# Kernel optimization log

Hardware: AMD Instinct MI355X
Metric: run time of the kernel (lower is better)

The kernel has to match this reference:

```python
import jax, jax.numpy as jnp
import numpy as np

EMB_DIM = 512
NUM_HEADS = 8
HEAD_DIM = EMB_DIM // NUM_HEADS


def setup_inputs() -> dict:
    key = jax.random.key(0)
    ks = jax.random.split(key, 8)
    B, S, D = 2, 192, EMB_DIM
    return {
        "q": jax.random.normal(ks[0], (B, S, D), dtype=jnp.float32),
        "k": jax.random.normal(ks[1], (B, S, D), dtype=jnp.float32),
        "l": jax.random.normal(ks[2], (B, S, D), dtype=jnp.float32),
        "v": jax.random.normal(ks[3], (B, S, D), dtype=jnp.float32),
        "Wq": jax.random.normal(ks[4], (D, D), dtype=jnp.float32) * (1.0 / np.sqrt(D)),
        "Wk": jax.random.normal(ks[5], (D, D), dtype=jnp.float32) * (1.0 / np.sqrt(D)),
        "Wv": jax.random.normal(ks[6], (D, D), dtype=jnp.float32) * (1.0 / np.sqrt(D)),
        "Wout": jax.random.normal(ks[7], (D, D), dtype=jnp.float32) * (1.0 / np.sqrt(D)),
    }


def _heads(x, W):
    # torch nn.Linear: x @ W.T ; then split heads -> (B, H, S, hd)
    B, S, D = x.shape
    y = x @ W.T
    return y.reshape(B, S, NUM_HEADS, HEAD_DIM).transpose(0, 2, 1, 3)


def reference(q, k, l, v, Wq, Wk, Wv, Wout):
    B, QS, D = q.shape
    KS, LS = k.shape[1], l.shape[1]
    qh = _heads(q, Wq)
    kh = _heads(k, Wk)
    lh = _heads(l, Wk)  # NOTE: original module projects l with self.key (faithful)
    vh = _heads(v, Wv)
    # rank-3 attention scores: (B, H, QS, KS, LS)
    scores = jnp.einsum('bhqe,bhke,bhle->bhqkl', qh, kh, lh) / jnp.sqrt(
        jnp.asarray(HEAD_DIM, dtype=q.dtype))
    # softmax jointly over (KS, LS)
    attn = jax.nn.softmax(scores.reshape(B, NUM_HEADS, QS, KS * LS), axis=-1)
    attn = attn.reshape(B, NUM_HEADS, QS, KS, LS)
    # vv[b,h,l,k,d] = v[b,h,k,d]; contract over k and l -> (B, QS, H, hd)
    attended = jnp.einsum('bhqkl,bhkd->bqhd', attn, vh)
    concatenated = attended.reshape(B, QS, EMB_DIM)
    return concatenated @ Wout.T
```

## Files before the change

kernel.cpp:

```cpp
#include <hip/hip_runtime.h>
#include <math.h>

#define BB 2
#define SS 192
#define DD 512
#define HH 8
#define HD 64
#define QCB 6
#define NQC (SS / QCB)
#define PROJ_N (BB*HH*SS*HD)
#define KLPAD (8 * 193 * 8)
#define SCL (0.125f * 1.44269504088896f)

typedef __attribute__((ext_vector_type(4))) float f32x4;
typedef _Float16 f16x8 __attribute__((ext_vector_type(8)));

__device__ __forceinline__ f16x8 cvt8_f16_rne(const float* g) {
    f16x8 r;
#pragma unroll
    for (int i = 0; i < 8; ++i) r[i] = (_Float16)g[i];
    return r;
}
__device__ __forceinline__ short f16s(float v) {
    return __builtin_bit_cast(short, (_Float16)v);
}

__global__ __launch_bounds__(256) void proj4_kernel(
    const float* __restrict__ xq, const float* __restrict__ xk,
    const float* __restrict__ xl, const float* __restrict__ xv,
    const float* __restrict__ Wq, const float* __restrict__ Wk,
    const float* __restrict__ Wv, float* __restrict__ vhp,
    short* __restrict__ qf16, short* __restrict__ khf16,
    short* __restrict__ lhf16, float* __restrict__ out) {
    const int p = blockIdx.z;
    const float* x = (p == 0) ? xq : (p == 1) ? xk : (p == 2) ? xl : xv;
    const float* W = (p == 0) ? Wq : (p == 3) ? Wv : Wk;

    __shared__ short Ahs[2][8 * 64 * 8];
    __shared__ short Bhs[2][8 * 64 * 8];

    const int t = threadIdx.x;

    {
        const int bid = (blockIdx.z * gridDim.y + blockIdx.y) * gridDim.x + blockIdx.x;
        for (int i = bid * 256 + t; i < BB * SS * DD; i += 192 * 256) out[i] = 0.f;
    }

    const int lane = t & 63, w = t >> 6;
    const int wr = w >> 1, wc = w & 1;
    const int c16 = lane & 15, q4 = lane >> 4;
    const int m0 = blockIdx.x * 64, n0 = blockIdx.y * 64;
    const int r = t >> 2, cc = t & 3;

    f32x4 acc[2][2];
#pragma unroll
    for (int a = 0; a < 2; ++a)
#pragma unroll
        for (int b = 0; b < 2; ++b) acc[a][b] = (f32x4){0.f, 0.f, 0.f, 0.f};

#define STAGE(kk, bf)                                                               \
    {                                                                               \
        _Pragma("unroll") for (int h2 = 0; h2 < 2; ++h2) {                          \
            const int ec = cc * 2 + h2;                                             \
            float a8[8], w8[8];                                                     \
            *(f32x4*)&a8[0] = *(const f32x4*)&x[(m0 + r) * 512 + (kk) + ec * 8];    \
            *(f32x4*)&a8[4] = *(const f32x4*)&x[(m0 + r) * 512 + (kk) + ec * 8 + 4];\
            *(f32x4*)&w8[0] = *(const f32x4*)&W[(n0 + r) * 512 + (kk) + ec * 8];    \
            *(f32x4*)&w8[4] = *(const f32x4*)&W[(n0 + r) * 512 + (kk) + ec * 8 + 4];\
            *(f16x8*)&Ahs[bf][(ec * 64 + r) * 8] = cvt8_f16_rne(a8);                \
            *(f16x8*)&Bhs[bf][(ec * 64 + r) * 8] = cvt8_f16_rne(w8);                \
        }                                                                           \
    }

    STAGE(0, 0)
    for (int s = 0; s < 8; ++s) {
        __syncthreads();
        if (s + 1 < 8) STAGE((s + 1) * 64, (s + 1) & 1)
        const int b = s & 1;
        f16x8 aH[2][2], bH[2][2];
#pragma unroll
        for (int mt = 0; mt < 2; ++mt) {
            const int row = wr * 32 + mt * 16 + c16;
            aH[mt][0] = *(const f16x8*)&Ahs[b][(q4 * 64 + row) * 8];
            aH[mt][1] = *(const f16x8*)&Ahs[b][((q4 + 4) * 64 + row) * 8];
        }
#pragma unroll
        for (int nt = 0; nt < 2; ++nt) {
            const int col = wc * 32 + nt * 16 + c16;
            bH[nt][0] = *(const f16x8*)&Bhs[b][(q4 * 64 + col) * 8];
            bH[nt][1] = *(const f16x8*)&Bhs[b][((q4 + 4) * 64 + col) * 8];
        }
#pragma unroll
        for (int mt = 0; mt < 2; ++mt)
#pragma unroll
            for (int nt = 0; nt < 2; ++nt) {
                acc[mt][nt] = __builtin_amdgcn_mfma_f32_16x16x32_f16(aH[mt][0], bH[nt][0], acc[mt][nt], 0, 0, 0);
                acc[mt][nt] = __builtin_amdgcn_mfma_f32_16x16x32_f16(aH[mt][1], bH[nt][1], acc[mt][nt], 0, 0, 0);
            }
    }
#undef STAGE

#pragma unroll
    for (int mt = 0; mt < 2; ++mt)
#pragma unroll
        for (int nt = 0; nt < 2; ++nt)
#pragma unroll
            for (int j = 0; j < 4; ++j) {
                const int n_row = m0 + wr * 32 + mt * 16 + q4 * 4 + j;
                const int col = n0 + wc * 32 + nt * 16 + c16;
                const int b = n_row / SS, s2 = n_row % SS;
                const int h = col >> 6, e = col & 63;
                const int bh = b * HH + h;
                const float v = acc[mt][nt][j];
                if (p == 3) {
                    vhp[(bh * SS + s2) * HD + e] = v;
                } else if (p == 0) {
                    qf16[(bh * SS + s2) * HD + e] = f16s(v * SCL);
                } else {
                    short* dst = (p == 1) ? khf16 : lhf16;
                    dst[bh * KLPAD + (e >> 3) * (193 * 8) + s2 * 8 + (e & 7)] = f16s(v);
                }
            }
}

__global__ __launch_bounds__(512, 4) void attn3d_mfma_kernel(
    const short* __restrict__ qf16, const short* __restrict__ khf16,
    const short* __restrict__ lhf16, const float* __restrict__ vh,
    const float* __restrict__ Wout, float* __restrict__ out) {
    __shared__ short Kf16[8][193][8];
    __shared__ short Lf16[8][193][8];
    __shared__ short qpk[QCB][8][8];
    __shared__ float partial[2][QCB][196];
    __shared__ float Wt[QCB][192];
    __shared__ float attd[16][72];
    __shared__ float zinv[QCB];

    const int blk = blockIdx.x;
    const int bh = blk >> 5, qc = blk & 31;
    const int t = threadIdx.x;
    const int lane = t & 63, w = t >> 6;
    const int lg = w >> 2, kg = w & 3;
    const int c = lane & 15, eh = lane >> 4;

    if (t < QCB * 8) {
        const int q = t >> 3, ecj = t & 7;
        *(f16x8*)&qpk[q][ecj][0] =
            *(const f16x8*)&qf16[(bh * SS + qc * QCB + q) * HD + ecj * 8];
    }
#pragma unroll
    for (int j = 0; j < 3; ++j) {
        const int cid = t + 512 * j;
        const int ec = cid / 192, k2 = cid - ec * 192;
        const int off = ec * (193 * 8) + k2 * 8;
        *(f16x8*)&(((short*)Kf16)[off]) = *(const f16x8*)&khf16[bh * KLPAD + off];
        *(f16x8*)&(((short*)Lf16)[off]) = *(const f16x8*)&lhf16[bh * KLPAD + off];
    }
    __syncthreads();

    for (int qpi = 0; qpi < 3; ++qpi) {
        const int qa = (qpi + w) % 3;
        const int qb = qa + 3;
        const f16x8 qaf0 = *(const f16x8*)&qpk[qa][eh][0];
        const f16x8 qaf1 = *(const f16x8*)&qpk[qa][4 + eh][0];
        const f16x8 qbf0 = *(const f16x8*)&qpk[qb][eh][0];
        const f16x8 qbf1 = *(const f16x8*)&qpk[qb][4 + eh][0];
        f16x8 Ba[3][2], Bb[3][2];
#pragma unroll
        for (int kt = 0; kt < 3; ++kt) {
            const int col = kg * 48 + kt * 16 + c;
            const f16x8 Kf0 = *(const f16x8*)&Kf16[eh][col][0];
            const f16x8 Kf1 = *(const f16x8*)&Kf16[4 + eh][col][0];
            Ba[kt][0] = Kf0 * qaf0;
            Ba[kt][1] = Kf1 * qaf1;
            Bb[kt][0] = Kf0 * qbf0;
            Bb[kt][1] = Kf1 * qbf1;
        }
        float ra0 = 0.f, ra1 = 0.f, ra2 = 0.f;
        float rb0 = 0.f, rb1 = 0.f, rb2 = 0.f;
#pragma unroll
        for (int lt = 0; lt < 6; ++lt) {
            const int row = lg * 96 + lt * 16 + c;
            const f16x8 A0 = *(const f16x8*)&Lf16[eh][row][0];
            const f16x8 A1 = *(const f16x8*)&Lf16[4 + eh][row][0];
            f32x4 a0 = (f32x4){0.f, 0.f, 0.f, 0.f};
            f32x4 a1 = (f32x4){0.f, 0.f, 0.f, 0.f};
            f32x4 a2 = (f32x4){0.f, 0.f, 0.f, 0.f};
            f32x4 b0 = (f32x4){0.f, 0.f, 0.f, 0.f};
            f32x4 b1 = (f32x4){0.f, 0.f, 0.f, 0.f};
            f32x4 b2 = (f32x4){0.f, 0.f, 0.f, 0.f};
            a0 = __builtin_amdgcn_mfma_f32_16x16x32_f16(A0, Ba[0][0], a0, 0, 0, 0);
            a1 = __builtin_amdgcn_mfma_f32_16x16x32_f16(A0, Ba[1][0], a1, 0, 0, 0);
            a2 = __builtin_amdgcn_mfma_f32_16x16x32_f16(A0, Ba[2][0], a2, 0, 0, 0);
            b0 = __builtin_amdgcn_mfma_f32_16x16x32_f16(A0, Bb[0][0], b0, 0, 0, 0);
            b1 = __builtin_amdgcn_mfma_f32_16x16x32_f16(A0, Bb[1][0], b1, 0, 0, 0);
            b2 = __builtin_amdgcn_mfma_f32_16x16x32_f16(A0, Bb[2][0], b2, 0, 0, 0);
            a0 = __builtin_amdgcn_mfma_f32_16x16x32_f16(A1, Ba[0][1], a0, 0, 0, 0);
            a1 = __builtin_amdgcn_mfma_f32_16x16x32_f16(A1, Ba[1][1], a1, 0, 0, 0);
            a2 = __builtin_amdgcn_mfma_f32_16x16x32_f16(A1, Ba[2][1], a2, 0, 0, 0);
            b0 = __builtin_amdgcn_mfma_f32_16x16x32_f16(A1, Bb[0][1], b0, 0, 0, 0);
            b1 = __builtin_amdgcn_mfma_f32_16x16x32_f16(A1, Bb[1][1], b1, 0, 0, 0);
            b2 = __builtin_amdgcn_mfma_f32_16x16x32_f16(A1, Bb[2][1], b2, 0, 0, 0);
            ra0 += (__builtin_amdgcn_exp2f(a0[0]) + __builtin_amdgcn_exp2f(a0[1])) +
                   (__builtin_amdgcn_exp2f(a0[2]) + __builtin_amdgcn_exp2f(a0[3]));
            ra1 += (__builtin_amdgcn_exp2f(a1[0]) + __builtin_amdgcn_exp2f(a1[1])) +
                   (__builtin_amdgcn_exp2f(a1[2]) + __builtin_amdgcn_exp2f(a1[3]));
            ra2 += (__builtin_amdgcn_exp2f(a2[0]) + __builtin_amdgcn_exp2f(a2[1])) +
                   (__builtin_amdgcn_exp2f(a2[2]) + __builtin_amdgcn_exp2f(a2[3]));
            rb0 += (__builtin_amdgcn_exp2f(b0[0]) + __builtin_amdgcn_exp2f(b0[1])) +
                   (__builtin_amdgcn_exp2f(b0[2]) + __builtin_amdgcn_exp2f(b0[3]));
            rb1 += (__builtin_amdgcn_exp2f(b1[0]) + __builtin_amdgcn_exp2f(b1[1])) +
                   (__builtin_amdgcn_exp2f(b1[2]) + __builtin_amdgcn_exp2f(b1[3]));
            rb2 += (__builtin_amdgcn_exp2f(b2[0]) + __builtin_amdgcn_exp2f(b2[1])) +
                   (__builtin_amdgcn_exp2f(b2[2]) + __builtin_amdgcn_exp2f(b2[3]));
        }
        ra0 += __shfl_xor(ra0, 16, 64);
        ra1 += __shfl_xor(ra1, 16, 64);
        ra2 += __shfl_xor(ra2, 16, 64);
        rb0 += __shfl_xor(rb0, 16, 64);
        rb1 += __shfl_xor(rb1, 16, 64);
        rb2 += __shfl_xor(rb2, 16, 64);
        ra0 += __shfl_xor(ra0, 32, 64);
        ra1 += __shfl_xor(ra1, 32, 64);
        ra2 += __shfl_xor(ra2, 32, 64);
        rb0 += __shfl_xor(rb0, 32, 64);
        rb1 += __shfl_xor(rb1, 32, 64);
        rb2 += __shfl_xor(rb2, 32, 64);
        if (eh == 0) {
            partial[lg][qa][kg * 48 + 0 * 16 + c] = ra0;
            partial[lg][qa][kg * 48 + 1 * 16 + c] = ra1;
            partial[lg][qa][kg * 48 + 2 * 16 + c] = ra2;
            partial[lg][qb][kg * 48 + 0 * 16 + c] = rb0;
            partial[lg][qb][kg * 48 + 1 * 16 + c] = rb1;
            partial[lg][qb][kg * 48 + 2 * 16 + c] = rb2;
        }
    }
    __syncthreads();

    for (int id = t; id < QCB * 192; id += 512) {
        const int q = id / 192, k = id - q * 192;
        Wt[q][k] = partial[0][q][k] + partial[1][q][k];
    }
    for (int id = t; id < 16 * 72; id += 512) ((float*)attd)[id] = 0.f;
    __syncthreads();

    if (w < QCB) {
        const int q = w;
        float z = Wt[q][lane] + Wt[q][lane + 64] + Wt[q][lane + 128];
#pragma unroll
        for (int off = 32; off >= 1; off >>= 1) z += __shfl_xor(z, off, 64);
        if (lane == 0) zinv[q] = 1.f / z;
    }
    __syncthreads();

    if (t < QCB * 64) {
        const int q = t >> 6, d = t & 63;
        const float* vp = vh + bh * SS * HD + d;
        float sum = 0.f;
        for (int k0 = 0; k0 < SS; k0 += 8) {
            float v8[8];
#pragma unroll
            for (int j = 0; j < 8; ++j) v8[j] = vp[(k0 + j) * HD];
#pragma unroll
            for (int j = 0; j < 8; ++j) sum = fmaf(Wt[q][k0 + j], v8[j], sum);
        }
        attd[q][d] = sum * zinv[q];
    }
    __syncthreads();

    const int b = bh >> 3, h = bh & 7;
    f16x8 Ae0, Ae1;
    {
        float a8[8];
        *(f32x4*)&a8[0] = *(const f32x4*)&attd[c][eh * 8];
        *(f32x4*)&a8[4] = *(const f32x4*)&attd[c][eh * 8 + 4];
        Ae0 = cvt8_f16_rne(a8);
        *(f32x4*)&a8[0] = *(const f32x4*)&attd[c][32 + eh * 8];
        *(f32x4*)&a8[4] = *(const f32x4*)&attd[c][32 + eh * 8 + 4];
        Ae1 = cvt8_f16_rne(a8);
    }
#pragma unroll
    for (int jt = 0; jt < 4; ++jt) {
        const int j = (w * 4 + jt) * 16 + c;
        const float* wp = &Wout[j * DD + h * HD];
        float b8[8];
        *(f32x4*)&b8[0] = *(const f32x4*)&wp[eh * 8];
        *(f32x4*)&b8[4] = *(const f32x4*)&wp[eh * 8 + 4];
        const f16x8 B0 = cvt8_f16_rne(b8);
        *(f32x4*)&b8[0] = *(const f32x4*)&wp[32 + eh * 8];
        *(f32x4*)&b8[4] = *(const f32x4*)&wp[32 + eh * 8 + 4];
        const f16x8 B1 = cvt8_f16_rne(b8);
        f32x4 oc = (f32x4){0.f, 0.f, 0.f, 0.f};
        oc = __builtin_amdgcn_mfma_f32_16x16x32_f16(Ae0, B0, oc, 0, 0, 0);
        oc = __builtin_amdgcn_mfma_f32_16x16x32_f16(Ae1, B1, oc, 0, 0, 0);
#pragma unroll
        for (int jj = 0; jj < 4; ++jj) {
            const int q = eh * 4 + jj;
            if (q < QCB)
                atomicAdd(&out[(b * SS + qc * QCB + q) * DD + (w * 4 + jt) * 16 + c], oc[jj]);
        }
    }
}

extern "C" void kernel_launch(void* const* d_in, const int* in_sizes, int n_in,
                              void* d_out, int out_size, void* d_ws, size_t ws_size,
                              hipStream_t stream) {
    (void)in_sizes; (void)n_in; (void)out_size; (void)ws_size;
    const float* q    = (const float*)d_in[0];
    const float* k    = (const float*)d_in[1];
    const float* l    = (const float*)d_in[2];
    const float* v    = (const float*)d_in[3];
    const float* Wq   = (const float*)d_in[4];
    const float* Wk   = (const float*)d_in[5];
    const float* Wv   = (const float*)d_in[6];
    const float* Wout = (const float*)d_in[7];
    float* out = (float*)d_out;

    float* ws    = (float*)d_ws;
    float* vhp   = ws;
    short* qf16  = (short*)(ws + PROJ_N);
    short* khf16 = qf16 + PROJ_N;
    short* lhf16 = khf16 + 16 * KLPAD;

    proj4_kernel<<<dim3(384 / 64, 512 / 64, 4), 256, 0, stream>>>(
        q, k, l, v, Wq, Wk, Wv, vhp, qf16, khf16, lhf16, out);
    attn3d_mfma_kernel<<<dim3(16 * NQC), 512, 0, stream>>>(
        qf16, khf16, lhf16, vhp, Wout, out);
}
```

Measured before the change: 42.38 us.

## Split projection K-reduction across two thread teams per block

The projection kernel now runs 512 threads per block, split into two 256-thread teams that each reduce half of the K=512 dimension with their own double-buffered shared tiles. Team 1 writes its partial accumulators to shared memory and team 0 adds them before the usual scatter to the head layouts. The aim is more parallelism and a shorter serial K loop for a grid of only 192 blocks, at the cost of extra shared memory, one additional barrier and the reduction step.

Result: no change. 41.91 us, median of 2 (-1.1%).

```diff
diff --git a/kernel.cpp b/kernel.cpp
--- a/kernel.cpp
+++ b/kernel.cpp
@@ -25,7 +25,7 @@
     return __builtin_bit_cast(short, (_Float16)v);
 }
 
-__global__ __launch_bounds__(256) void proj4_kernel(
+__global__ __launch_bounds__(512) void proj4_kernel(
     const float* __restrict__ xq, const float* __restrict__ xk,
     const float* __restrict__ xl, const float* __restrict__ xv,
     const float* __restrict__ Wq, const float* __restrict__ Wk,
@@ -36,21 +36,24 @@
     const float* x = (p == 0) ? xq : (p == 1) ? xk : (p == 2) ? xl : xv;
     const float* W = (p == 0) ? Wq : (p == 3) ? Wv : Wk;
 
-    __shared__ short Ahs[2][8 * 64 * 8];
-    __shared__ short Bhs[2][8 * 64 * 8];
+    __shared__ short Ahs[2][2][8 * 64 * 8];
+    __shared__ short Bhs[2][2][8 * 64 * 8];
+    __shared__ float accs[64][65];
 
     const int t = threadIdx.x;
 
     {
         const int bid = (blockIdx.z * gridDim.y + blockIdx.y) * gridDim.x + blockIdx.x;
-        for (int i = bid * 256 + t; i < BB * SS * DD; i += 192 * 256) out[i] = 0.f;
-    }
-
-    const int lane = t & 63, w = t >> 6;
-    const int wr = w >> 1, wc = w & 1;
+        for (int i = bid * 512 + t; i < BB * SS * DD; i += 192 * 512) out[i] = 0.f;
+    }
+
+    const int team = t >> 8, tt = t & 255;
+    const int lane = tt & 63, w4 = tt >> 6;
+    const int wr = w4 >> 1, wc = w4 & 1;
     const int c16 = lane & 15, q4 = lane >> 4;
     const int m0 = blockIdx.x * 64, n0 = blockIdx.y * 64;
-    const int r = t >> 2, cc = t & 3;
+    const int r = tt >> 2, cc = tt & 3;
+    const int kbase = team * 256;
 
     f32x4 acc[2][2];
 #pragma unroll
@@ -67,28 +70,28 @@
             *(f32x4*)&a8[4] = *(const f32x4*)&x[(m0 + r) * 512 + (kk) + ec * 8 + 4];\
             *(f32x4*)&w8[0] = *(const f32x4*)&W[(n0 + r) * 512 + (kk) + ec * 8];    \
             *(f32x4*)&w8[4] = *(const f32x4*)&W[(n0 + r) * 512 + (kk) + ec * 8 + 4];\
-            *(f16x8*)&Ahs[bf][(ec * 64 + r) * 8] = cvt8_f16_rne(a8);                \
-            *(f16x8*)&Bhs[bf][(ec * 64 + r) * 8] = cvt8_f16_rne(w8);                \
+            *(f16x8*)&Ahs[team][bf][(ec * 64 + r) * 8] = cvt8_f16_rne(a8);          \
+            *(f16x8*)&Bhs[team][bf][(ec * 64 + r) * 8] = cvt8_f16_rne(w8);          \
         }                                                                           \
     }
 
-    STAGE(0, 0)
-    for (int s = 0; s < 8; ++s) {
+    STAGE(kbase, 0)
+    for (int s = 0; s < 4; ++s) {
         __syncthreads();
-        if (s + 1 < 8) STAGE((s + 1) * 64, (s + 1) & 1)
+        if (s + 1 < 4) STAGE(kbase + (s + 1) * 64, (s + 1) & 1)
         const int b = s & 1;
         f16x8 aH[2][2], bH[2][2];
 #pragma unroll
         for (int mt = 0; mt < 2; ++mt) {
             const int row = wr * 32 + mt * 16 + c16;
-            aH[mt][0] = *(const f16x8*)&Ahs[b][(q4 * 64 + row) * 8];
-            aH[mt][1] = *(const f16x8*)&Ahs[b][((q4 + 4) * 64 + row) * 8];
+            aH[mt][0] = *(const f16x8*)&Ahs[team][b][(q4 * 64 + row) * 8];
+            aH[mt][1] = *(const f16x8*)&Ahs[team][b][((q4 + 4) * 64 + row) * 8];
         }
 #pragma unroll
         for (int nt = 0; nt < 2; ++nt) {
             const int col = wc * 32 + nt * 16 + c16;
-            bH[nt][0] = *(const f16x8*)&Bhs[b][(q4 * 64 + col) * 8];
-            bH[nt][1] = *(const f16x8*)&Bhs[b][((q4 + 4) * 64 + col) * 8];
+            bH[nt][0] = *(const f16x8*)&Bhs[team][b][(q4 * 64 + col) * 8];
+            bH[nt][1] = *(const f16x8*)&Bhs[team][b][((q4 + 4) * 64 + col) * 8];
         }
 #pragma unroll
         for (int mt = 0; mt < 2; ++mt)
@@ -100,27 +103,44 @@
     }
 #undef STAGE
 
-#pragma unroll
-    for (int mt = 0; mt < 2; ++mt)
-#pragma unroll
-        for (int nt = 0; nt < 2; ++nt)
-#pragma unroll
-            for (int j = 0; j < 4; ++j) {
-                const int n_row = m0 + wr * 32 + mt * 16 + q4 * 4 + j;
-                const int col = n0 + wc * 32 + nt * 16 + c16;
-                const int b = n_row / SS, s2 = n_row % SS;
-                const int h = col >> 6, e = col & 63;
-                const int bh = b * HH + h;
-                const float v = acc[mt][nt][j];
-                if (p == 3) {
-                    vhp[(bh * SS + s2) * HD + e] = v;
-                } else if (p == 0) {
-                    qf16[(bh * SS + s2) * HD + e] = f16s(v * SCL);
-                } else {
-                    short* dst = (p == 1) ? khf16 : lhf16;
-                    dst[bh * KLPAD + (e >> 3) * (193 * 8) + s2 * 8 + (e & 7)] = f16s(v);
+    if (team == 1) {
+#pragma unroll
+        for (int mt = 0; mt < 2; ++mt)
+#pragma unroll
+            for (int nt = 0; nt < 2; ++nt)
+#pragma unroll
+                for (int j = 0; j < 4; ++j) {
+                    const int row = wr * 32 + mt * 16 + q4 * 4 + j;
+                    const int col = wc * 32 + nt * 16 + c16;
+                    accs[row][col] = acc[mt][nt][j];
                 }
-            }
+    }
+    __syncthreads();
+    if (team == 0) {
+#pragma unroll
+        for (int mt = 0; mt < 2; ++mt)
+#pragma unroll
+            for (int nt = 0; nt < 2; ++nt)
+#pragma unroll
+                for (int j = 0; j < 4; ++j) {
+                    const int row = wr * 32 + mt * 16 + q4 * 4 + j;
+                    const int col = wc * 32 + nt * 16 + c16;
+                    const float v = acc[mt][nt][j] + accs[row][col];
+                    const int n_row = m0 + row;
+                    const int jcol = n0 + col;
+                    const int b = n_row / SS, s2 = n_row % SS;
+                    const int h = jcol >> 6, e = jcol & 63;
+                    const int bh = b * HH + h;
+                    if (p == 3) {
+                        vhp[(bh * SS + s2) * HD + e] = v;
+                    } else if (p == 0) {
+                        qf16[(bh * SS + s2) * HD + e] = f16s(v * SCL);
+                    } else {
+                        short* dst = (p == 1) ? khf16 : lhf16;
+                        dst[bh * KLPAD + (e >> 3) * (193 * 8) + s2 * 8 + (e & 7)] = f16s(v);
+                    }
+                }
+    }
 }
 
 __global__ __launch_bounds__(512, 4) void attn3d_mfma_kernel(
@@ -321,7 +341,7 @@
     short* khf16 = qf16 + PROJ_N;
     short* lhf16 = khf16 + 16 * KLPAD;
 
-    proj4_kernel<<<dim3(384 / 64, 512 / 64, 4), 256, 0, stream>>>(
+    proj4_kernel<<<dim3(384 / 64, 512 / 64, 4), 512, 0, stream>>>(
         q, k, l, v, Wq, Wk, Wv, vhp, qf16, khf16, lhf16, out);
     attn3d_mfma_kernel<<<dim3(16 * NQC), 512, 0, stream>>>(
         qf16, khf16, lhf16, vhp, Wout, out);
```
